# Kernel tuning notes

Hardware: AMD Instinct MI355X
Metric: run time of the kernel (lower is better)

Reference implementation:

```python
import jax, jax.numpy as jnp
import numpy as np

N_NODES = 4096
N_SUBS = 1024
NUM_FEATURES = 128
HIDDEN = 512
NHEADS = 8
DHEAD = HIDDEN // NHEADS
NUM_LAYERS = 2
EDGE_PROB = 0.01
NEG_INF = -1e9


def _make_adj(key, n, p):
    a = (jax.random.uniform(key, (n, n)) < p).astype(jnp.float32)
    return jnp.maximum(a, jnp.eye(n, dtype=jnp.float32))  # self-loops


def setup_inputs() -> dict:
    key = jax.random.key(0)
    ks = jax.random.split(key, 12)
    x = jax.random.normal(ks[0], (N_NODES, NUM_FEATURES), dtype=jnp.float32)
    adj_node = _make_adj(ks[1], N_NODES, EDGE_PROB)
    adj_substation = _make_adj(ks[2], N_SUBS, 4 * EDGE_PROB)
    seg_ids = jnp.sort(jax.random.randint(ks[3], (N_NODES,), 0, N_SUBS, dtype=jnp.int32))
    s = 0.05
    lin_w = jax.random.normal(ks[4], (NUM_FEATURES, HIDDEN), dtype=jnp.float32) * s
    lin_b = jnp.zeros((HIDDEN,), dtype=jnp.float32)
    node_W = jax.random.normal(ks[5], (NUM_LAYERS, HIDDEN, HIDDEN), dtype=jnp.float32) * s
    node_asrc = jax.random.normal(ks[6], (NUM_LAYERS, NHEADS, DHEAD), dtype=jnp.float32) * s
    node_adst = jax.random.normal(ks[7], (NUM_LAYERS, NHEADS, DHEAD), dtype=jnp.float32) * s
    sub_W = jax.random.normal(ks[8], (NUM_LAYERS, HIDDEN, HIDDEN), dtype=jnp.float32) * s
    sub_asrc = jax.random.normal(ks[9], (NUM_LAYERS, NHEADS, DHEAD), dtype=jnp.float32) * s
    sub_adst = jax.random.normal(ks[10], (NUM_LAYERS, NHEADS, DHEAD), dtype=jnp.float32) * s
    return {"x": x, "adj_node": adj_node, "adj_substation": adj_substation,
            "seg_ids": seg_ids, "lin_w": lin_w, "lin_b": lin_b,
            "node_W": node_W, "node_asrc": node_asrc, "node_adst": node_adst,
            "sub_W": sub_W, "sub_asrc": sub_asrc, "sub_adst": sub_adst}


def _gat_layer(h, adj, W, a_src, a_dst):
    # h: [N, F]; adj: [N, N]; W: [F, F]; a_src/a_dst: [H, Dh]
    n = h.shape[0]
    Wh = (h @ W).reshape(n, NHEADS, DHEAD)               # [N, H, Dh]
    f_src = jnp.einsum('nhd,hd->hn', Wh, a_src)          # [H, N]
    f_dst = jnp.einsum('nhd,hd->hn', Wh, a_dst)          # [H, N]
    e = jax.nn.leaky_relu(f_src[:, :, None] + f_dst[:, None, :], 0.2)  # [H, N, N]
    e = jnp.where(adj[None] > 0, e, NEG_INF)
    alpha = jax.nn.softmax(e, axis=-1)                   # [H, N, N]
    out = jnp.einsum('hij,jhd->ihd', alpha, Wh).reshape(n, NHEADS * DHEAD)
    return jax.nn.elu(out)


def _stacked_gats(h, adj, Ws, asrcs, adsts):
    # Faithful to the source bug: x is never rebound, each layer sees the
    # original input; the last layer's output is returned.
    out = h
    for i in range(Ws.shape[0]):
        out = _gat_layer(h, adj, Ws[i], asrcs[i], adsts[i])
    return out


def _pool_mean(h, seg_ids, num_segments):
    sums = jax.ops.segment_sum(h, seg_ids, num_segments=num_segments)
    counts = jax.ops.segment_sum(jnp.ones((h.shape[0], 1), h.dtype), seg_ids,
                                 num_segments=num_segments)
    return sums / jnp.maximum(counts, 1.0)


def reference(x, adj_node, adj_substation, seg_ids, lin_w, lin_b,
              node_W, node_asrc, node_adst, sub_W, sub_asrc, sub_adst):
    h = x @ lin_w + lin_b                                  # [N, HIDDEN]
    h = _stacked_gats(h, adj_node, node_W, node_asrc, node_adst)
    s = _pool_mean(h, seg_ids, N_SUBS)                     # [S, HIDDEN]
    s = _stacked_gats(s, adj_substation, sub_W, sub_asrc, sub_adst)
    return s
```

## Files before the change

### kernel.cpp

```cpp
#include <hip/hip_runtime.h>
#include <hip/hip_bf16.h>
#include <math.h>

#define N_NODES 4096
#define N_SUBS  1024
#define NFEAT   128
#define HIDDEN  512
#define NHEADS  8
#define DHEAD   64
#define CAP     128
#define ROWG    4

__global__ __launch_bounds__(256) void extract_both(const float* __restrict__ adj_n,
                                                    const float* __restrict__ adj_s,
                                                    int* __restrict__ cnt_n,
                                                    int* __restrict__ nbr_n,
                                                    int* __restrict__ cnt_s,
                                                    int* __restrict__ nbr_s) {
    const int w = threadIdx.x >> 6;
    const int lane = threadIdx.x & 63;
    const float* adj;
    int N, row;
    int* cnt;
    int* nbr;
    if (blockIdx.x < N_NODES / 4) {
        adj = adj_n; N = N_NODES; cnt = cnt_n; nbr = nbr_n;
        row = blockIdx.x * 4 + w;
    } else {
        adj = adj_s; N = N_SUBS; cnt = cnt_s; nbr = nbr_s;
        row = (blockIdx.x - N_NODES / 4) * 4 + w;
    }
    const float4* rowp = (const float4*)(adj + (size_t)row * N);
    int* nrow = nbr + (row << 7);
    const int n4 = N >> 2;
    int c = 0;
    const unsigned long long below = (1ull << lane) - 1ull;
    for (int c4 = lane; c4 < n4; c4 += 64) {
        const float4 v = rowp[c4];
        const int col = c4 << 2;
        unsigned long long m;
        bool p;
        p = v.x > 0.0f; m = __ballot(p);
        if (p) { int q = c + __popcll(m & below); if (q < CAP) nrow[q] = col; }
        c += __popcll(m);
        p = v.y > 0.0f; m = __ballot(p);
        if (p) { int q = c + __popcll(m & below); if (q < CAP) nrow[q] = col + 1; }
        c += __popcll(m);
        p = v.z > 0.0f; m = __ballot(p);
        if (p) { int q = c + __popcll(m & below); if (q < CAP) nrow[q] = col + 2; }
        c += __popcll(m);
        p = v.w > 0.0f; m = __ballot(p);
        if (p) { int q = c + __popcll(m & below); if (q < CAP) nrow[q] = col + 3; }
        c += __popcll(m);
    }
    if (lane == 0) cnt[row] = c < CAP ? c : CAP;
}

#define BM 64
#define BN 64
#define BK 16
__global__ __launch_bounds__(256) void gemm_f32(const float* __restrict__ A,
                                                const float* __restrict__ B,
                                                const float* __restrict__ bias,
                                                float* __restrict__ C,
                                                int M, int N, int K, int k_chunk,
                                                const float* __restrict__ asrc,
                                                const float* __restrict__ adst,
                                                float* __restrict__ fs,
                                                float* __restrict__ fd) {
    __shared__ float As[BK][BM + 4];
    __shared__ float Bs[BK][BN + 4];
    const int tid = threadIdx.x;
    const int bm = blockIdx.y * BM;
    const int bn = blockIdx.x * BN;
    const int k_start = blockIdx.z * k_chunk;
    const int k_end = (k_start + k_chunk) < K ? (k_start + k_chunk) : K;
    float* Cw = C + (size_t)blockIdx.z * M * N;
    const int tr = tid >> 4;
    const int tc = tid & 15;
    const int am = tid >> 2;
    const int ak4 = (tid & 3) * 4;
    const int bk = tid >> 4;
    const int bn0 = (tid & 15) * 4;
    float acc[4][4] = {};
    for (int k0 = k_start; k0 < k_end; k0 += BK) {
        const float4 va = *(const float4*)&A[(size_t)(bm + am) * K + k0 + ak4];
        const float4 vb = *(const float4*)&B[(size_t)(k0 + bk) * N + bn + bn0];
        As[ak4 + 0][am] = va.x;
        As[ak4 + 1][am] = va.y;
        As[ak4 + 2][am] = va.z;
        As[ak4 + 3][am] = va.w;
        *(float4*)&Bs[bk][bn0] = vb;
        __syncthreads();
#pragma unroll
        for (int k = 0; k < BK; k++) {
            const float4 a4 = *(const float4*)&As[k][tr * 4];
            const float4 b4 = *(const float4*)&Bs[k][tc * 4];
            const float a[4] = {a4.x, a4.y, a4.z, a4.w};
            const float b[4] = {b4.x, b4.y, b4.z, b4.w};
#pragma unroll
            for (int i = 0; i < 4; i++)
#pragma unroll
                for (int j = 0; j < 4; j++)
                    acc[i][j] += a[i] * b[j];
        }
        __syncthreads();
    }
#pragma unroll
    for (int i = 0; i < 4; i++) {
        const int m = bm + tr * 4 + i;
        if (bias) {
            const float4 bv = *(const float4*)&bias[bn + tc * 4];
            acc[i][0] += bv.x; acc[i][1] += bv.y; acc[i][2] += bv.z; acc[i][3] += bv.w;
        }
        float4 o = {acc[i][0], acc[i][1], acc[i][2], acc[i][3]};
        *(float4*)&Cw[(size_t)m * N + bn + tc * 4] = o;
    }
    if (asrc) {
        const int h = blockIdx.x;
        const float4 as4 = *(const float4*)&asrc[h * DHEAD + tc * 4];
        const float4 ad4 = *(const float4*)&adst[h * DHEAD + tc * 4];
#pragma unroll
        for (int i = 0; i < 4; i++) {
            float vs = acc[i][0] * as4.x + acc[i][1] * as4.y +
                       acc[i][2] * as4.z + acc[i][3] * as4.w;
            float vd = acc[i][0] * ad4.x + acc[i][1] * ad4.y +
                       acc[i][2] * ad4.z + acc[i][3] * ad4.w;
#pragma unroll
            for (int off = 1; off < 16; off <<= 1) {
                vs += __shfl_xor(vs, off, 64);
                vd += __shfl_xor(vd, off, 64);
            }
            if (tc == 0) {
                const int m = bm + tr * 4 + i;
                fs[h * M + m] = vs;
                fd[h * M + m] = vd;
            }
        }
    }
}

__global__ __launch_bounds__(256) void reduce_both(const float* __restrict__ p1,
                                                   float* __restrict__ o1,
                                                   int len1, int nz1,
                                                   const float* __restrict__ p2,
                                                   float* __restrict__ o2,
                                                   int len2, int nz2,
                                                   int blocks1) {
    if ((int)blockIdx.x < blocks1) {
        const int i = blockIdx.x * 256 + threadIdx.x;
        if (i < len1) {
            float s = 0.0f;
            for (int z = 0; z < nz1; z++) s += p1[(size_t)z * len1 + i];
            o1[i] = s;
        }
    } else {
        const int i = (blockIdx.x - blocks1) * 256 + threadIdx.x;
        if (i < len2) {
            float s = 0.0f;
            for (int z = 0; z < nz2; z++) s += p2[(size_t)z * len2 + i];
            o2[i] = s;
        }
    }
}

__global__ __launch_bounds__(256) void gemv_bias_part(const float* __restrict__ lin_b,
                                                      const float* __restrict__ W1,
                                                      float* __restrict__ part) {
    const int n = blockIdx.x * 256 + threadIdx.x;
    const int z = blockIdx.y;
    const int k0 = z * (HIDDEN / 16);
    float s = 0.0f;
#pragma unroll 4
    for (int k = k0; k < k0 + HIDDEN / 16; k++)
        s += lin_b[k] * W1[(size_t)k * HIDDEN + n];
    part[z * HIDDEN + n] = s;
}

__global__ __launch_bounds__(512) void reduce_fsfd(const float* __restrict__ part,
                                                   float* __restrict__ wh,
                                                   const float* __restrict__ asrc,
                                                   const float* __restrict__ adst,
                                                   float* __restrict__ fs,
                                                   float* __restrict__ fd,
                                                   int M, int nz) {
    const int n = blockIdx.x;
    const int tid = threadIdx.x;
    float v = 0.0f;
    for (int z = 0; z < nz; z++)
        v += part[((size_t)z * M + n) * HIDDEN + tid];
    wh[(size_t)n * HIDDEN + tid] = v;
    const int h = tid >> 6;
    const int d = tid & 63;
    float vs = v * asrc[h * DHEAD + d];
    float vd = v * adst[h * DHEAD + d];
#pragma unroll
    for (int off = 32; off >= 1; off >>= 1) {
        vs += __shfl_xor(vs, off, 64);
        vd += __shfl_xor(vd, off, 64);
    }
    if (d == 0) {
        fs[h * M + n] = vs;
        fd[h * M + n] = vd;
    }
}

__global__ __launch_bounds__(512) void gat_agg(const float* __restrict__ Wh,
                                               const float* __restrict__ fs,
                                               const float* __restrict__ fd,
                                               const int* __restrict__ cnt,
                                               const int* __restrict__ nbr,
                                               float* __restrict__ out, int N,
                                               int jlo, int jhi,
                                               int first, int last) {
    __shared__ int snbr[CAP];
    __shared__ float ex[NHEADS][CAP + 1];
    __shared__ float sacc[ROWG][HIDDEN];
    const int i = blockIdx.x;
    const int tid = threadIdx.x;
    int C = cnt[i];
    C = C < CAP ? C : CAP;
    for (int k = tid; k < C; k += 512) snbr[k] = nbr[(i << 7) + k];
    __syncthreads();
    const int klo = __syncthreads_count((tid < C) && (snbr[tid] < jlo));
    const int khi = __syncthreads_count((tid < C) && (snbr[tid] < jhi));
    {
        const int h = tid >> 6;
        const int lane = tid & 63;
        const float fsi = fs[h * N + i];
        const float* __restrict__ fdh = fd + h * N;
        float m = -1e30f;
        for (int k = lane; k < C; k += 64) {
            float e = fsi + fdh[snbr[k]];
            e = e > 0.0f ? e : 0.2f * e;
            ex[h][k] = e;
            m = fmaxf(m, e);
        }
#pragma unroll
        for (int off = 32; off >= 1; off >>= 1) m = fmaxf(m, __shfl_xor(m, off, 64));
        float ssum = 0.0f;
        for (int k = lane; k < C; k += 64) {
            float v = __expf(ex[h][k] - m);
            ex[h][k] = v;
            ssum += v;
        }
#pragma unroll
        for (int off = 32; off >= 1; off >>= 1) ssum += __shfl_xor(ssum, off, 64);
        const float inv = 1.0f / ssum;
        for (int k = lane; k < C; k += 64) ex[h][k] *= inv;
    }
    __syncthreads();
    const int g = tid >> 7;
    const int t = tid & 127;
    const int hh = t >> 4;
    float4 acc = {0.f, 0.f, 0.f, 0.f};
    int k = klo + g;
    for (; k + ROWG < khi; k += 2 * ROWG) {
        const int j0 = snbr[k];
        const int j1 = snbr[k + ROWG];
        const float a0 = ex[hh][k];
        const float a1 = ex[hh][k + ROWG];
        const float4 w0 = *(const float4*)&Wh[(size_t)j0 * HIDDEN + 4 * t];
        const float4 w1 = *(const float4*)&Wh[(size_t)j1 * HIDDEN + 4 * t];
        acc.x += a0 * w0.x + a1 * w1.x;
        acc.y += a0 * w0.y + a1 * w1.y;
        acc.z += a0 * w0.z + a1 * w1.z;
        acc.w += a0 * w0.w + a1 * w1.w;
    }
    if (k < khi) {
        const int j0 = snbr[k];
        const float a0 = ex[hh][k];
        const float4 w0 = *(const float4*)&Wh[(size_t)j0 * HIDDEN + 4 * t];
        acc.x += a0 * w0.x; acc.y += a0 * w0.y;
        acc.z += a0 * w0.z; acc.w += a0 * w0.w;
    }
    *(float4*)&sacc[g][4 * t] = acc;
    __syncthreads();
    if (g == 0) {
        float4 r = acc;
#pragma unroll
        for (int gg = 1; gg < ROWG; gg++) {
            const float4 o = *(const float4*)&sacc[gg][4 * t];
            r.x += o.x; r.y += o.y; r.z += o.z; r.w += o.w;
        }
        float4* op = (float4*)&out[(size_t)i * HIDDEN + 4 * t];
        if (!first) {
            const float4 p = *op;
            r.x += p.x; r.y += p.y; r.z += p.z; r.w += p.w;
        }
        if (last) {
            r.x = r.x > 0.0f ? r.x : __expf(r.x) - 1.0f;
            r.y = r.y > 0.0f ? r.y : __expf(r.y) - 1.0f;
            r.z = r.z > 0.0f ? r.z : __expf(r.z) - 1.0f;
            r.w = r.w > 0.0f ? r.w : __expf(r.w) - 1.0f;
        }
        *op = r;
    }
}

__global__ __launch_bounds__(512) void pool_kernel(const float* __restrict__ hin,
                                                   const int* __restrict__ seg,
                                                   float* __restrict__ sout) {
    const int s = blockIdx.x;
    const int d = threadIdx.x;
    int lo = 0, hi = N_NODES;
    while (lo < hi) { int mid = (lo + hi) >> 1; if (seg[mid] < s) lo = mid + 1; else hi = mid; }
    const int start = lo;
    hi = N_NODES;
    while (lo < hi) { int mid = (lo + hi) >> 1; if (seg[mid] < s + 1) lo = mid + 1; else hi = mid; }
    const int end = lo;
    float acc = 0.0f;
    for (int r = start; r < end; r++) acc += hin[(size_t)r * HIDDEN + d];
    const int c = end - start;
    sout[(size_t)s * HIDDEN + d] = acc / (c > 0 ? (float)c : 1.0f);
}

extern "C" void kernel_launch(void* const* d_in, const int* in_sizes, int n_in,
                              void* d_out, int out_size, void* d_ws, size_t ws_size,
                              hipStream_t stream) {
    const float* x        = (const float*)d_in[0];
    const float* adj_node = (const float*)d_in[1];
    const float* adj_sub  = (const float*)d_in[2];
    const int*   seg_ids  = (const int*)d_in[3];
    const float* lin_w    = (const float*)d_in[4];
    const float* lin_b    = (const float*)d_in[5];
    const float* node_W1    = (const float*)d_in[6]  + HIDDEN * HIDDEN;
    const float* node_asrc1 = (const float*)d_in[7]  + NHEADS * DHEAD;
    const float* node_adst1 = (const float*)d_in[8]  + NHEADS * DHEAD;
    const float* sub_W1     = (const float*)d_in[9]  + HIDDEN * HIDDEN;
    const float* sub_asrc1  = (const float*)d_in[10] + NHEADS * DHEAD;
    const float* sub_adst1  = (const float*)d_in[11] + NHEADS * DHEAD;
    float* out = (float*)d_out;

    char* ws = (char*)d_ws;
    float* bufA  = (float*)(ws);
    float* bufB  = (float*)(ws + (size_t)8 * 1024 * 1024);
    float* fs_n  = (float*)(ws + (size_t)16 * 1024 * 1024);
    float* fd_n  = fs_n + NHEADS * N_NODES;
    float* fs_s  = fd_n + NHEADS * N_NODES;
    float* fd_s  = fs_s + NHEADS * N_SUBS;
    int*   cnt_n = (int*)(fd_s + NHEADS * N_SUBS);
    int*   cnt_s = cnt_n + N_NODES;
    int*   nbr_n = cnt_s + N_SUBS;
    int*   nbr_s = nbr_n + N_NODES * CAP;

    float* Wpart = bufB;
    float* Wfuse = bufB + 16 * NFEAT * HIDDEN;
    float* bpart = Wfuse + NFEAT * HIDDEN;
    float* bias2 = bpart + 16 * HIDDEN;
    float* wh_n  = bufA;
    float* gatom = bufB;
    float* sp    = bufA;
    float* Spart = bufB;
    float* wh_s  = bufA + (size_t)N_SUBS * HIDDEN;

    extract_both<<<N_NODES / 4 + N_SUBS / 4, 256, 0, stream>>>(
        adj_node, adj_sub, cnt_n, nbr_n, cnt_s, nbr_s);
    gemm_f32<<<dim3(HIDDEN / BN, NFEAT / BM, 16), 256, 0, stream>>>(
        lin_w, node_W1, nullptr, Wpart, NFEAT, HIDDEN, HIDDEN, HIDDEN / 16,
        nullptr, nullptr, nullptr, nullptr);
    gemv_bias_part<<<dim3(HIDDEN / 256, 16), 256, 0, stream>>>(lin_b, node_W1, bpart);
    reduce_both<<<NFEAT * HIDDEN / 256 + 2, 256, 0, stream>>>(
        Wpart, Wfuse, NFEAT * HIDDEN, 16, bpart, bias2, HIDDEN, 16,
        NFEAT * HIDDEN / 256);
    gemm_f32<<<dim3(HIDDEN / BN, N_NODES / BM, 1), 256, 0, stream>>>(
        x, Wfuse, bias2, wh_n, N_NODES, HIDDEN, NFEAT, NFEAT,
        node_asrc1, node_adst1, fs_n, fd_n);
    gat_agg<<<N_NODES, 512, 0, stream>>>(wh_n, fs_n, fd_n, cnt_n, nbr_n,
                                         gatom, N_NODES, 0, N_NODES / 2, 1, 0);
    gat_agg<<<N_NODES, 512, 0, stream>>>(wh_n, fs_n, fd_n, cnt_n, nbr_n,
                                         gatom, N_NODES, N_NODES / 2, N_NODES, 0, 1);
    pool_kernel<<<N_SUBS, 512, 0, stream>>>(gatom, seg_ids, sp);
    gemm_f32<<<dim3(HIDDEN / BN, N_SUBS / BM, 4), 256, 0, stream>>>(
        sp, sub_W1, nullptr, Spart, N_SUBS, HIDDEN, HIDDEN, HIDDEN / 4,
        nullptr, nullptr, nullptr, nullptr);
    reduce_fsfd<<<N_SUBS, 512, 0, stream>>>(Spart, wh_s, sub_asrc1, sub_adst1,
                                            fs_s, fd_s, N_SUBS, 4);
    gat_agg<<<N_SUBS, 512, 0, stream>>>(wh_s, fs_s, fd_s, cnt_s, nbr_s,
                                        out, N_SUBS, 0, N_SUBS, 1, 1);
}
```

Baseline: 232.1 us.

## Merge split GAT aggregation passes, fold bias GEMV into GEMM, nontemporal adjacency loads

Replaces the two column-range gat_agg launches with a single pass over all neighbours, removing the read-modify-write of the partial output. Widens the neighbour gather unroll from 2 to 4 rows per step. Folds the lin_b @ W1 bias GEMV into an extra block row of the first GEMM launch, and switches adjacency reads in the extraction kernel to nontemporal loads. Together these cut launch count and redundant global traffic. The single-pass gather loses whatever cache locality the column split was meant to give on the Wh reads.

```diff
diff --git a/kernel.cpp b/kernel.cpp
--- a/kernel.cpp
+++ b/kernel.cpp
@@ -10,6 +10,8 @@
 #define DHEAD   64
 #define CAP     128
 #define ROWG    4
+
+typedef float vfloat4 __attribute__((ext_vector_type(4)));
 
 __global__ __launch_bounds__(256) void extract_both(const float* __restrict__ adj_n,
                                                     const float* __restrict__ adj_s,
@@ -30,13 +32,13 @@
         adj = adj_s; N = N_SUBS; cnt = cnt_s; nbr = nbr_s;
         row = (blockIdx.x - N_NODES / 4) * 4 + w;
     }
-    const float4* rowp = (const float4*)(adj + (size_t)row * N);
+    const vfloat4* rowp = (const vfloat4*)(adj + (size_t)row * N);
     int* nrow = nbr + (row << 7);
     const int n4 = N >> 2;
     int c = 0;
     const unsigned long long below = (1ull << lane) - 1ull;
     for (int c4 = lane; c4 < n4; c4 += 64) {
-        const float4 v = rowp[c4];
+        const vfloat4 v = __builtin_nontemporal_load(&rowp[c4]);
         const int col = c4 << 2;
         unsigned long long m;
         bool p;
@@ -67,7 +69,9 @@
                                                 const float* __restrict__ asrc,
                                                 const float* __restrict__ adst,
                                                 float* __restrict__ fs,
-                                                float* __restrict__ fd) {
+                                                float* __restrict__ fd,
+                                                const float* __restrict__ lin_b,
+                                                float* __restrict__ bias_part) {
     __shared__ float As[BK][BM + 4];
     __shared__ float Bs[BK][BN + 4];
     const int tid = threadIdx.x;
@@ -75,6 +79,23 @@
     const int bn = blockIdx.x * BN;
     const int k_start = blockIdx.z * k_chunk;
     const int k_end = (k_start + k_chunk) < K ? (k_start + k_chunk) : K;
+    if (lin_b && blockIdx.y == gridDim.y - 1) {
+        const int q = tid >> 6;
+        const int n = tid & 63;
+        const int sub = k_chunk >> 2;
+        const int kb = k_start + q * sub;
+        float s = 0.0f;
+        for (int k = 0; k < sub; k++)
+            s += lin_b[kb + k] * B[(size_t)(kb + k) * N + bn + n];
+        float* red = (float*)As;
+        red[q * 64 + n] = s;
+        __syncthreads();
+        if (q == 0) {
+            s = red[n] + red[64 + n] + red[128 + n] + red[192 + n];
+            bias_part[blockIdx.z * N + bn + n] = s;
+        }
+        return;
+    }
     float* Cw = C + (size_t)blockIdx.z * M * N;
     const int tr = tid >> 4;
     const int tc = tid & 15;
@@ -164,19 +185,6 @@
     }
 }
 
-__global__ __launch_bounds__(256) void gemv_bias_part(const float* __restrict__ lin_b,
-                                                      const float* __restrict__ W1,
-                                                      float* __restrict__ part) {
-    const int n = blockIdx.x * 256 + threadIdx.x;
-    const int z = blockIdx.y;
-    const int k0 = z * (HIDDEN / 16);
-    float s = 0.0f;
-#pragma unroll 4
-    for (int k = k0; k < k0 + HIDDEN / 16; k++)
-        s += lin_b[k] * W1[(size_t)k * HIDDEN + n];
-    part[z * HIDDEN + n] = s;
-}
-
 __global__ __launch_bounds__(512) void reduce_fsfd(const float* __restrict__ part,
                                                    float* __restrict__ wh,
                                                    const float* __restrict__ asrc,
@@ -210,9 +218,7 @@
                                                const float* __restrict__ fd,
                                                const int* __restrict__ cnt,
                                                const int* __restrict__ nbr,
-                                               float* __restrict__ out, int N,
-                                               int jlo, int jhi,
-                                               int first, int last) {
+                                               float* __restrict__ out, int N) {
     __shared__ int snbr[CAP];
     __shared__ float ex[NHEADS][CAP + 1];
     __shared__ float sacc[ROWG][HIDDEN];
@@ -222,8 +228,6 @@
     C = C < CAP ? C : CAP;
     for (int k = tid; k < C; k += 512) snbr[k] = nbr[(i << 7) + k];
     __syncthreads();
-    const int klo = __syncthreads_count((tid < C) && (snbr[tid] < jlo));
-    const int khi = __syncthreads_count((tid < C) && (snbr[tid] < jhi));
     {
         const int h = tid >> 6;
         const int lane = tid & 63;
@@ -254,20 +258,26 @@
     const int t = tid & 127;
     const int hh = t >> 4;
     float4 acc = {0.f, 0.f, 0.f, 0.f};
-    int k = klo + g;
-    for (; k + ROWG < khi; k += 2 * ROWG) {
+    int k = g;
+    for (; k + 3 * ROWG < C; k += 4 * ROWG) {
         const int j0 = snbr[k];
         const int j1 = snbr[k + ROWG];
+        const int j2 = snbr[k + 2 * ROWG];
+        const int j3 = snbr[k + 3 * ROWG];
         const float a0 = ex[hh][k];
         const float a1 = ex[hh][k + ROWG];
+        const float a2 = ex[hh][k + 2 * ROWG];
+        const float a3 = ex[hh][k + 3 * ROWG];
         const float4 w0 = *(const float4*)&Wh[(size_t)j0 * HIDDEN + 4 * t];
         const float4 w1 = *(const float4*)&Wh[(size_t)j1 * HIDDEN + 4 * t];
-        acc.x += a0 * w0.x + a1 * w1.x;
-        acc.y += a0 * w0.y + a1 * w1.y;
-        acc.z += a0 * w0.z + a1 * w1.z;
-        acc.w += a0 * w0.w + a1 * w1.w;
-    }
-    if (k < khi) {
+        const float4 w2 = *(const float4*)&Wh[(size_t)j2 * HIDDEN + 4 * t];
+        const float4 w3 = *(const float4*)&Wh[(size_t)j3 * HIDDEN + 4 * t];
+        acc.x += a0 * w0.x + a1 * w1.x + a2 * w2.x + a3 * w3.x;
+        acc.y += a0 * w0.y + a1 * w1.y + a2 * w2.y + a3 * w3.y;
+        acc.z += a0 * w0.z + a1 * w1.z + a2 * w2.z + a3 * w3.z;
+        acc.w += a0 * w0.w + a1 * w1.w + a2 * w2.w + a3 * w3.w;
+    }
+    for (; k < C; k += ROWG) {
         const int j0 = snbr[k];
         const float a0 = ex[hh][k];
         const float4 w0 = *(const float4*)&Wh[(size_t)j0 * HIDDEN + 4 * t];
@@ -283,18 +293,11 @@
             const float4 o = *(const float4*)&sacc[gg][4 * t];
             r.x += o.x; r.y += o.y; r.z += o.z; r.w += o.w;
         }
-        float4* op = (float4*)&out[(size_t)i * HIDDEN + 4 * t];
-        if (!first) {
-            const float4 p = *op;
-            r.x += p.x; r.y += p.y; r.z += p.z; r.w += p.w;
-        }
-        if (last) {
-            r.x = r.x > 0.0f ? r.x : __expf(r.x) - 1.0f;
-            r.y = r.y > 0.0f ? r.y : __expf(r.y) - 1.0f;
-            r.z = r.z > 0.0f ? r.z : __expf(r.z) - 1.0f;
-            r.w = r.w > 0.0f ? r.w : __expf(r.w) - 1.0f;
-        }
-        *op = r;
+        r.x = r.x > 0.0f ? r.x : __expf(r.x) - 1.0f;
+        r.y = r.y > 0.0f ? r.y : __expf(r.y) - 1.0f;
+        r.z = r.z > 0.0f ? r.z : __expf(r.z) - 1.0f;
+        r.w = r.w > 0.0f ? r.w : __expf(r.w) - 1.0f;
+        *(float4*)&out[(size_t)i * HIDDEN + 4 * t] = r;
     }
 }
 
@@ -356,26 +359,23 @@
 
     extract_both<<<N_NODES / 4 + N_SUBS / 4, 256, 0, stream>>>(
         adj_node, adj_sub, cnt_n, nbr_n, cnt_s, nbr_s);
-    gemm_f32<<<dim3(HIDDEN / BN, NFEAT / BM, 16), 256, 0, stream>>>(
+    gemm_f32<<<dim3(HIDDEN / BN, NFEAT / BM + 1, 16), 256, 0, stream>>>(
         lin_w, node_W1, nullptr, Wpart, NFEAT, HIDDEN, HIDDEN, HIDDEN / 16,
-        nullptr, nullptr, nullptr, nullptr);
-    gemv_bias_part<<<dim3(HIDDEN / 256, 16), 256, 0, stream>>>(lin_b, node_W1, bpart);
+        nullptr, nullptr, nullptr, nullptr, lin_b, bpart);
     reduce_both<<<NFEAT * HIDDEN / 256 + 2, 256, 0, stream>>>(
         Wpart, Wfuse, NFEAT * HIDDEN, 16, bpart, bias2, HIDDEN, 16,
         NFEAT * HIDDEN / 256);
     gemm_f32<<<dim3(HIDDEN / BN, N_NODES / BM, 1), 256, 0, stream>>>(
         x, Wfuse, bias2, wh_n, N_NODES, HIDDEN, NFEAT, NFEAT,
-        node_asrc1, node_adst1, fs_n, fd_n);
+        node_asrc1, node_adst1, fs_n, fd_n, nullptr, nullptr);
     gat_agg<<<N_NODES, 512, 0, stream>>>(wh_n, fs_n, fd_n, cnt_n, nbr_n,
-                                         gatom, N_NODES, 0, N_NODES / 2, 1, 0);
-    gat_agg<<<N_NODES, 512, 0, stream>>>(wh_n, fs_n, fd_n, cnt_n, nbr_n,
-                                         gatom, N_NODES, N_NODES / 2, N_NODES, 0, 1);
+                                         gatom, N_NODES);
     pool_kernel<<<N_SUBS, 512, 0, stream>>>(gatom, seg_ids, sp);
     gemm_f32<<<dim3(HIDDEN / BN, N_SUBS / BM, 4), 256, 0, stream>>>(
         sp, sub_W1, nullptr, Spart, N_SUBS, HIDDEN, HIDDEN, HIDDEN / 4,
-        nullptr, nullptr, nullptr, nullptr);
+        nullptr, nullptr, nullptr, nullptr, nullptr, nullptr);
     reduce_fsfd<<<N_SUBS, 512, 0, stream>>>(Spart, wh_s, sub_asrc1, sub_adst1,
                                             fs_s, fd_s, N_SUBS, 4);
     gat_agg<<<N_SUBS, 512, 0, stream>>>(wh_s, fs_s, fd_s, cnt_s, nbr_s,
-                                        out, N_SUBS, 0, N_SUBS, 1, 1);
-}
+                                        out, N_SUBS);
+}
```

New measurement: 220.5 us. -5.0%, faster.
